# Optimization experiments

Measured on AMD Instinct MI355X. Metric: run time of the kernel, lower is better.

The kernel has to match this reference:

```python
import jax, jax.numpy as jnp
import numpy as np

N = 100000
E = 1600000
F_IN = 32   # node_features
F_H = 32    # filters
F_OUT = 4


def setup_inputs() -> dict:
    key = jax.random.key(0)
    ks = jax.random.split(key, 24)
    inp = {
        'x': jax.random.normal(ks[0], (N, F_IN), dtype=jnp.float32),
        'edge_index': jax.random.randint(ks[1], (2, E), 0, N, dtype=jnp.int64),
        'edge_weight': jax.random.uniform(ks[2], (E,), dtype=jnp.float32),
        'H': jax.random.normal(ks[3], (N, F_H), dtype=jnp.float32),
    }
    # ChebConv params: W[k] for k in {0,1} (K=2), bias per conv.
    def cheb_params(kw, kb, fin):
        s = 1.0 / np.sqrt(fin)
        W = jax.random.uniform(kw, (2, fin, F_H), jnp.float32, -s, s)
        b = jax.random.uniform(kb, (F_H,), jnp.float32, -s, s)
        return W, b
    names = ['xz', 'hz', 'xr', 'hr', 'xh', 'hh']
    fins = [F_IN, F_H, F_IN, F_H, F_IN, F_H]
    for i, (nm, fin) in enumerate(zip(names, fins)):
        W, b = cheb_params(ks[4 + 2 * i], ks[5 + 2 * i], fin)
        inp['W' + nm] = W
        inp['b' + nm] = b
    s = 1.0 / np.sqrt(F_H)
    inp['lin_w'] = jax.random.uniform(ks[20], (F_H, F_OUT), jnp.float32, -s, s)
    inp['lin_b'] = jax.random.uniform(ks[21], (F_OUT,), jnp.float32, -s, s)
    return inp


def _cheb(x, src, dst, nw, W, b):
    # ChebConv, K=2, sym norm, lambda_max=2 => L_hat = -D^{-1/2} A D^{-1/2}
    # (diagonal of scaled Laplacian cancels exactly: 1 - 1 = 0).
    tx1 = -jax.ops.segment_sum(nw[:, None] * x[src], dst, num_segments=N)
    return x @ W[0] + tx1 @ W[1] + b


def reference(x, edge_index, edge_weight, H,
              Wxz, bxz, Whz, bhz, Wxr, bxr, Whr, bhr, Wxh, bxh, Whh, bhh,
              lin_w, lin_b):
    src, dst = edge_index[0], edge_index[1]
    # remove_self_loops equivalent: zero out self-loop weights
    w = jnp.where(src == dst, 0.0, edge_weight)
    deg = jax.ops.segment_sum(w, src, num_segments=N)
    dinv = jnp.where(deg > 0, jax.lax.rsqrt(jnp.maximum(deg, 1e-30)), 0.0)
    nw = dinv[src] * w * dinv[dst]  # per-edge sym-normalized weight

    Z = jax.nn.sigmoid(_cheb(x, src, dst, nw, Wxz, bxz) +
                       _cheb(H, src, dst, nw, Whz, bhz))
    R = jax.nn.sigmoid(_cheb(x, src, dst, nw, Wxr, bxr) +
                       _cheb(H, src, dst, nw, Whr, bhr))
    H_tilde = jnp.tanh(_cheb(x, src, dst, nw, Wxh, bxh) +
                       _cheb(H * R, src, dst, nw, Whh, bhh))
    h = Z * H + (1.0 - Z) * H_tilde
    out = jax.nn.relu(h) @ lin_w + lin_b
    return (out, h)
```

## Files before the change

kernel.cpp:

```cpp
#include <hip/hip_runtime.h>
#include <hip/hip_bf16.h>
#include <hip/hip_fp16.h>

typedef __hip_bfloat16 bf16;
typedef __attribute__((ext_vector_type(8))) short bf16x8;
typedef __attribute__((ext_vector_type(4))) float f32x4;

#define NN   100000
#define EE   1600000
#define FH   32
#define FOUT 4
#define NBD  782
#define NBS  196
#define CAPB 2432
#define CAPS 8960
#define CAP  64
#define BINBLK 256
#define BINTHR 1024
#define EPB  6250
#define MFMA16(a, b, c) __builtin_amdgcn_mfma_f32_16x16x32_bf16(a, b, c, 0, 0, 0)

__device__ __forceinline__ float b2f(bf16 v) { return __bfloat162float(v); }

__device__ __forceinline__ float ldf(const void* p, int i, int f32) {
    return f32 ? ((const float*)p)[i] : b2f(((const bf16*)p)[i]);
}
__device__ __forceinline__ int ldi(const void* p, int i, int i64f) {
    return i64f ? (int)(((const long long*)p)[i]) : ((const int*)p)[i];
}
__device__ __forceinline__ void stf(void* p, int i, int f32, float v) {
    if (f32) ((float*)p)[i] = v;
    else     ((bf16*)p)[i] = __float2bfloat16(v);
}
__device__ __forceinline__ float h2f(unsigned short u) {
    return __half2float(__ushort_as_half(u));
}
__device__ __forceinline__ unsigned short f2h16(float v) {
    return __half_as_ushort(__float2half(v));
}
__device__ __forceinline__ short f2bf(float v) {
    unsigned u = __float_as_uint(v);
    return (short)((u + 0x7FFFu + ((u >> 16) & 1u)) >> 16);
}
__device__ __forceinline__ unsigned q8(float v) {
    int q = (int)rintf(v * 16.f) + 128;
    q = q < 0 ? 0 : (q > 255 ? 255 : q);
    return (unsigned)q;
}
__device__ __forceinline__ float ub(unsigned w, int k) {
    return (float)((w >> (k * 8)) & 0xFFu);
}
__device__ __forceinline__ float4 bfly_g(float4 v) {
    v.x += __shfl_xor(v.x, 8);  v.y += __shfl_xor(v.y, 8);
    v.z += __shfl_xor(v.z, 8);  v.w += __shfl_xor(v.w, 8);
    v.x += __shfl_xor(v.x, 16); v.y += __shfl_xor(v.y, 16);
    v.z += __shfl_xor(v.z, 16); v.w += __shfl_xor(v.w, 16);
    return v;
}
__device__ __forceinline__ bf16x8 bfragT(const short* __restrict__ wt, int idx) {
    return *(const bf16x8*)(wt + idx);
}

__global__ __launch_bounds__(256) void k_detect(const void* __restrict__ x,
                                                const void* __restrict__ ei,
                                                int* __restrict__ flg,
                                                int* __restrict__ binCur,
                                                int* __restrict__ binCurS) {
    __shared__ int s_f32[256], s_oddnz[256];
    int t = threadIdx.x;
    for (int i = t; i < NBD; i += 256) binCur[i] = i * CAPB;
    for (int i = t; i < NBS; i += 256) binCurS[i] = i * CAPS;
    float v = b2f(((const bf16*)x)[t]);
    s_f32[t] = (!isfinite(v)) || (fabsf(v) > 100.f);
    int w32 = ((const int*)ei)[t];
    s_oddnz[t] = ((t & 1) && (w32 != 0)) ? 1 : 0;
    __syncthreads();
    if (t == 0) {
        int f32 = 0, oddnz = 0;
        for (int i = 0; i < 256; i++) { f32 |= s_f32[i]; oddnz |= s_oddnz[i]; }
        flg[0] = f32;
        flg[1] = oddnz ? 0 : 1;
    }
}

__global__ __launch_bounds__(256) void k_prepw(
    const void* __restrict__ W0, const void* __restrict__ W1,
    const void* __restrict__ W2, const void* __restrict__ W3,
    const void* __restrict__ W4, const void* __restrict__ W5,
    const int* __restrict__ flg, short* __restrict__ wt) {
    int i = blockIdx.x * 256 + threadIdx.x;
    if (i >= 6 * 2048) return;
    int mat = i >> 11;
    int r = i & 2047;
    int cheb = r >> 10, k = (r >> 5) & 31, n = r & 31;
    const void* W = (mat == 0) ? W0 : (mat == 1) ? W1 : (mat == 2) ? W2
                  : (mat == 3) ? W3 : (mat == 4) ? W4 : W5;
    wt[(((mat << 1) + cheb) << 10) + n * 32 + k] = f2bf(ldf(W, r, flg[0]));
}

__global__ __launch_bounds__(256) void k_pack(const void* __restrict__ x,
                                              const void* __restrict__ H,
                                              const int* __restrict__ flg,
                                              unsigned* __restrict__ xh,
                                              unsigned short* __restrict__ xh8) {
    int i = blockIdx.x * 256 + threadIdx.x;
    if (i >= NN * FH) return;
    int f32 = flg[0];
    float xv = ldf(x, i, f32);
    float hv = ldf(H, i, f32);
    xh[i] = ((unsigned)f2h16(hv) << 16) | f2h16(xv);
    xh8[i] = (unsigned short)((q8(hv) << 8) | q8(xv));
}

__global__ __launch_bounds__(BINTHR) void k_bin(const void* __restrict__ ei,
                                                const void* __restrict__ ew,
                                                const int* __restrict__ flg,
                                                int* __restrict__ binCur,
                                                int* __restrict__ binCurS,
                                                int2* __restrict__ dstRec,
                                                int* __restrict__ srcRec) {
    __shared__ int hD[NBD], bD[NBD], lofD[NBD];
    __shared__ int hS[NBS], bS[NBS], lofS[NBS];
    __shared__ int sc[BINTHR];
    __shared__ int2 stD[EPB];
    __shared__ int  stS[EPB];
    int t = threadIdx.x;
    for (int i = t; i < NBD; i += BINTHR) hD[i] = 0;
    for (int i = t; i < NBS; i += BINTHR) hS[i] = 0;
    __syncthreads();
    int e0 = blockIdx.x * EPB;
    int e1 = e0 + EPB; if (e1 > EE) e1 = EE;
    int f32 = flg[0], i64 = flg[1];
    for (int e = e0 + t; e < e1; e += BINTHR) {
        int s = ldi(ei, e, i64);
        int d = ldi(ei, EE + e, i64);
        atomicAdd(&hD[d >> 7], 1);
        atomicAdd(&hS[s >> 9], 1);
    }
    __syncthreads();
    for (int i = t; i < NBD; i += BINTHR)
        bD[i] = (hD[i] > 0) ? atomicAdd(&binCur[i], hD[i]) : 0;
    for (int i = t; i < NBS; i += BINTHR)
        bS[i] = (hS[i] > 0) ? atomicAdd(&binCurS[i], hS[i]) : 0;
    int vD = (t < NBD) ? hD[t] : 0;
    sc[t] = vD;
    __syncthreads();
    for (int ofs = 1; ofs < BINTHR; ofs <<= 1) {
        int u = (t >= ofs) ? sc[t - ofs] : 0;
        __syncthreads();
        sc[t] += u;
        __syncthreads();
    }
    if (t < NBD) { lofD[t] = sc[t] - vD; hD[t] = 0; }
    __syncthreads();
    int vS = (t < NBS) ? hS[t] : 0;
    sc[t] = vS;
    __syncthreads();
    for (int ofs = 1; ofs < BINTHR; ofs <<= 1) {
        int u = (t >= ofs) ? sc[t - ofs] : 0;
        __syncthreads();
        sc[t] += u;
        __syncthreads();
    }
    if (t < NBS) { lofS[t] = sc[t] - vS; hS[t] = 0; }
    __syncthreads();
    for (int e = e0 + t; e < e1; e += BINTHR) {
        int s = ldi(ei, e, i64);
        int d = ldi(ei, EE + e, i64);
        float w = (s == d) ? 0.f : ldf(ew, e, f32);
        int wh = (int)(f2h16(w) & 0x7FFFu);
        int bd = d >> 7, bs = s >> 9;
        int rd = atomicAdd(&hD[bd], 1);
        int rs = atomicAdd(&hS[bs], 1);
        stD[lofD[bd] + rd] = make_int2((int)(((unsigned)s << 15) | wh),
                                       (bd << 8) | (d & 127));
        stS[lofS[bs] + rs] = (int)(((unsigned)bs << 24) |
                                   ((unsigned)(s & 511) << 15) | (unsigned)wh);
    }
    __syncthreads();
    int tot = e1 - e0;
    for (int i = t; i < tot; i += BINTHR) {
        int2 r = stD[i];
        int bin = ((unsigned)r.y) >> 8;
        int g = bD[bin] + (i - lofD[bin]);
        if (g < (bin + 1) * CAPB) dstRec[g] = make_int2(r.x, r.y & 127);
        int u = stS[i];
        int sbin = ((unsigned)u) >> 24;
        int gs = bS[sbin] + (i - lofS[sbin]);
        if (gs < (sbin + 1) * CAPS) srcRec[gs] = u & 0xFFFFFF;
    }
}

__global__ __launch_bounds__(256) void k_fillb(const int* __restrict__ binCur,
                                               const int2* __restrict__ dstRec,
                                               int* __restrict__ cursor,
                                               int* __restrict__ ell) {
    __shared__ int lCur[128];
    __shared__ int lEll[128 * CAP];
    int b = blockIdx.x, t = threadIdx.x;
    if (t < 128) lCur[t] = 0;
    __syncthreads();
    int cnt = binCur[b] - b * CAPB;
    if (cnt > CAPB) cnt = CAPB;
    for (int i = t; i < cnt; i += 256) {
        int2 r = dstRec[b * CAPB + i];
        int slot = atomicAdd(&lCur[r.y], 1);
        if (slot < CAP) lEll[r.y * CAP + slot] = r.x;
    }
    __syncthreads();
    int nodeBase = b * 128;
    for (int i = t; i < 128 * CAP; i += 256) {
        int node = nodeBase + (i >> 6);
        if (node < NN && (i & 63) < lCur[i >> 6])
            ell[(size_t)node * CAP + (i & (CAP - 1))] = lEll[i];
    }
    if (t < 128 && nodeBase + t < NN) {
        int c = lCur[t]; if (c > CAP) c = CAP;
        cursor[nodeBase + t] = c;
    }
}

__global__ __launch_bounds__(256) void k_degb(const int* __restrict__ binCurS,
                                              const int* __restrict__ srcRec,
                                              float* __restrict__ dinv) {
    __shared__ float lDeg[512];
    int b = blockIdx.x, t = threadIdx.x;
    lDeg[t] = 0.f; lDeg[t + 256] = 0.f;
    __syncthreads();
    int cnt = binCurS[b] - b * CAPS;
    if (cnt > CAPS) cnt = CAPS;
    for (int i = t; i < cnt; i += 256) {
        int r = srcRec[b * CAPS + i];
        atomicAdd(&lDeg[(r >> 15) & 511], h2f((unsigned short)(r & 0x7FFF)));
    }
    __syncthreads();
    #pragma unroll
    for (int k = 0; k < 2; k++) {
        int li = t + k * 256;
        int node = b * 512 + li;
        if (node < NN) {
            float dv = lDeg[li];
            dinv[node] = (dv > 0.f) ? rsqrtf(dv) : 0.f;
        }
    }
}

__global__ __launch_bounds__(256) void k_gather1(const int* __restrict__ cursor,
                                                 const int* __restrict__ ell,
                                                 const float* __restrict__ dinv,
                                                 const unsigned short* __restrict__ xh8,
                                                 unsigned* __restrict__ axah) {
    int t = threadIdx.x;
    int node = blockIdx.x * 8 + (t >> 5);
    if (node >= NN) return;
    int f = t & 31;
    int g = f >> 3, c = f & 7;
    int cnt = cursor[node];
    size_t base = (size_t)node * CAP;
    float4 ax = {0.f, 0.f, 0.f, 0.f}, ah = {0.f, 0.f, 0.f, 0.f};
    float cs = 0.f;
    for (int j = 0; j < cnt; j += 16) {
        int wrd[4]; float cf[4]; uint2 pv[4];
        #pragma unroll
        for (int u = 0; u < 4; u++) {
            int jj = j + u * 4 + g;
            wrd[u] = (jj < cnt) ? ell[base + jj] : 0;
        }
        #pragma unroll
        for (int u = 0; u < 4; u++) {
            int s = ((unsigned)wrd[u]) >> 15;
            cf[u] = dinv[s] * h2f((unsigned short)(wrd[u] & 0x7FFF));
            pv[u] = ((const uint2*)xh8)[s * 8 + c];
        }
        #pragma unroll
        for (int u = 0; u < 4; u++) {
            cs += cf[u];
            ax.x += cf[u] * ub(pv[u].x, 0);
            ah.x += cf[u] * ub(pv[u].x, 1);
            ax.y += cf[u] * ub(pv[u].x, 2);
            ah.y += cf[u] * ub(pv[u].x, 3);
            ax.z += cf[u] * ub(pv[u].y, 0);
            ah.z += cf[u] * ub(pv[u].y, 1);
            ax.w += cf[u] * ub(pv[u].y, 2);
            ah.w += cf[u] * ub(pv[u].y, 3);
        }
    }
    ax = bfly_g(ax); ah = bfly_g(ah);
    cs += __shfl_xor(cs, 8);
    cs += __shfl_xor(cs, 16);
    if (g == 0) {
        float dd = -dinv[node];
        float bias = 8.f * cs;
        uint4 o;
        o.x = ((unsigned)f2h16(dd * (ah.x * 0.0625f - bias)) << 16)
            | f2h16(dd * (ax.x * 0.0625f - bias));
        o.y = ((unsigned)f2h16(dd * (ah.y * 0.0625f - bias)) << 16)
            | f2h16(dd * (ax.y * 0.0625f - bias));
        o.z = ((unsigned)f2h16(dd * (ah.z * 0.0625f - bias)) << 16)
            | f2h16(dd * (ax.z * 0.0625f - bias));
        o.w = ((unsigned)f2h16(dd * (ah.w * 0.0625f - bias)) << 16)
            | f2h16(dd * (ax.w * 0.0625f - bias));
        ((uint4*)(axah + (size_t)node * FH))[c] = o;
    }
}

__global__ __launch_bounds__(256) void k_zr_mfma(
    const unsigned* __restrict__ xh, const unsigned* __restrict__ axah,
    const int* __restrict__ flg, const short* __restrict__ wt,
    const void* __restrict__ bxz, const void* __restrict__ bhz,
    const void* __restrict__ bxr, const void* __restrict__ bhr,
    float* __restrict__ Z, unsigned short* __restrict__ hr16) {
    int t = threadIdx.x;
    int lane = t & 63, wv = t >> 6;
    int f32 = flg[0];
    int c = lane & 15, quad = lane >> 4, kb = quad * 8;
    int nodeBase = blockIdx.x * 64 + wv * 16;
    int nm = nodeBase + c; if (nm >= NN) nm = NN - 1;

    bf16x8 fx, fHH, fAX, fAH;
    {
        const uint4* p = (const uint4*)(xh + (size_t)nm * FH + kb);
        uint4 a = p[0], b = p[1];
        unsigned wd[8] = {a.x, a.y, a.z, a.w, b.x, b.y, b.z, b.w};
        #pragma unroll
        for (int j = 0; j < 8; j++) {
            fx[j]  = f2bf(h2f((unsigned short)(wd[j] & 0xFFFF)));
            fHH[j] = f2bf(h2f((unsigned short)(wd[j] >> 16)));
        }
    }
    {
        const uint4* p = (const uint4*)(axah + (size_t)nm * FH + kb);
        uint4 a = p[0], b = p[1];
        unsigned wd[8] = {a.x, a.y, a.z, a.w, b.x, b.y, b.z, b.w};
        #pragma unroll
        for (int j = 0; j < 8; j++) {
            fAX[j] = f2bf(h2f((unsigned short)(wd[j] & 0xFFFF)));
            fAH[j] = f2bf(h2f((unsigned short)(wd[j] >> 16)));
        }
    }

    float bz0 = ldf(bxz, c, f32) + ldf(bhz, c, f32);
    float bz1 = ldf(bxz, c + 16, f32) + ldf(bhz, c + 16, f32);
    float br0 = ldf(bxr, c, f32) + ldf(bhr, c, f32);
    float br1 = ldf(bxr, c + 16, f32) + ldf(bhr, c + 16, f32);
    f32x4 az0 = {bz0, bz0, bz0, bz0}, az1 = {bz1, bz1, bz1, bz1};
    f32x4 ar0 = {br0, br0, br0, br0}, ar1 = {br1, br1, br1, br1};

    int i0 = c * 32 + kb;
    int i1 = (c + 16) * 32 + kb;
    az0 = MFMA16(fx,  bfragT(wt, 0 * 1024 + i0), az0);
    az0 = MFMA16(fAX, bfragT(wt, 1 * 1024 + i0), az0);
    az0 = MFMA16(fHH, bfragT(wt, 2 * 1024 + i0), az0);
    az0 = MFMA16(fAH, bfragT(wt, 3 * 1024 + i0), az0);
    az1 = MFMA16(fx,  bfragT(wt, 0 * 1024 + i1), az1);
    az1 = MFMA16(fAX, bfragT(wt, 1 * 1024 + i1), az1);
    az1 = MFMA16(fHH, bfragT(wt, 2 * 1024 + i1), az1);
    az1 = MFMA16(fAH, bfragT(wt, 3 * 1024 + i1), az1);
    ar0 = MFMA16(fx,  bfragT(wt, 4 * 1024 + i0), ar0);
    ar0 = MFMA16(fAX, bfragT(wt, 5 * 1024 + i0), ar0);
    ar0 = MFMA16(fHH, bfragT(wt, 6 * 1024 + i0), ar0);
    ar0 = MFMA16(fAH, bfragT(wt, 7 * 1024 + i0), ar0);
    ar1 = MFMA16(fx,  bfragT(wt, 4 * 1024 + i1), ar1);
    ar1 = MFMA16(fAX, bfragT(wt, 5 * 1024 + i1), ar1);
    ar1 = MFMA16(fHH, bfragT(wt, 6 * 1024 + i1), ar1);
    ar1 = MFMA16(fAH, bfragT(wt, 7 * 1024 + i1), ar1);

    #pragma unroll
    for (int tl = 0; tl < 2; tl++) {
        f32x4 az = tl ? az1 : az0, ar = tl ? ar1 : ar0;
        int f = c + 16 * tl;
        #pragma unroll
        for (int r = 0; r < 4; r++) {
            int node = nodeBase + quad * 4 + r;
            if (node < NN) {
                float zv = 1.f / (1.f + expf(-az[r]));
                float rv = 1.f / (1.f + expf(-ar[r]));
                float Hv = h2f((unsigned short)(xh[(size_t)node * FH + f] >> 16));
                Z[(size_t)node * FH + f] = zv;
                hr16[(size_t)node * FH + f] = f2h16(Hv * rv);
            }
        }
    }
}

__global__ __launch_bounds__(256) void k_gather2(const int* __restrict__ cursor,
                                                 const int* __restrict__ ell,
                                                 const float* __restrict__ dinv,
                                                 const unsigned short* __restrict__ hr16,
                                                 unsigned short* __restrict__ ahr16) {
    int t = threadIdx.x;
    int node = blockIdx.x * 8 + (t >> 5);
    if (node >= NN) return;
    int f = t & 31;
    int g = f >> 3, c = f & 7;
    int cnt = cursor[node];
    size_t base = (size_t)node * CAP;
    float4 acc = {0.f, 0.f, 0.f, 0.f};
    for (int j = 0; j < cnt; j += 8) {
        int jj0 = j + g, jj1 = j + 4 + g;
        int wrd0 = (jj0 < cnt) ? ell[base + jj0] : 0;
        int wrd1 = (jj1 < cnt) ? ell[base + jj1] : 0;
        int s0 = ((unsigned)wrd0) >> 15;
        int s1 = ((unsigned)wrd1) >> 15;
        float c0 = dinv[s0] * h2f((unsigned short)(wrd0 & 0x7FFF));
        float c1 = dinv[s1] * h2f((unsigned short)(wrd1 & 0x7FFF));
        ushort4 h0 = ((const ushort4*)hr16)[s0 * 8 + c];
        ushort4 h1 = ((const ushort4*)hr16)[s1 * 8 + c];
        acc.x += c0 * h2f(h0.x) + c1 * h2f(h1.x);
        acc.y += c0 * h2f(h0.y) + c1 * h2f(h1.y);
        acc.z += c0 * h2f(h0.z) + c1 * h2f(h1.z);
        acc.w += c0 * h2f(h0.w) + c1 * h2f(h1.w);
    }
    acc = bfly_g(acc);
    if (g == 0) {
        float dd = -dinv[node];
        ushort4 o = {f2h16(dd * acc.x), f2h16(dd * acc.y),
                     f2h16(dd * acc.z), f2h16(dd * acc.w)};
        ((ushort4*)(ahr16 + (size_t)node * FH))[c] = o;
    }
}

__global__ __launch_bounds__(256) void k_final_mfma(
    const unsigned* __restrict__ xh, const unsigned* __restrict__ axah,
    const int* __restrict__ flg, const short* __restrict__ wt,
    const float* __restrict__ Z, const unsigned short* __restrict__ hr16,
    const unsigned short* __restrict__ ahr16,
    const void* __restrict__ bxh, const void* __restrict__ bhh,
    const void* __restrict__ lin_w, const void* __restrict__ lin_b,
    void* __restrict__ out) {
    __shared__ float srh[64][FH];
    __shared__ float slw[FH * FOUT];
    __shared__ float slb[FOUT];

    int t = threadIdx.x;
    int lane = t & 63, wv = t >> 6;
    int f32 = flg[0];
    int c = lane & 15, quad = lane >> 4, kb = quad * 8;
    int nodeBase = blockIdx.x * 64 + wv * 16;
    int nm = nodeBase + c; if (nm >= NN) nm = NN - 1;

    if (t < FH * FOUT) slw[t] = ldf(lin_w, t, f32);
    if (t < FOUT) slb[t] = ldf(lin_b, t, f32);

    bf16x8 fx, fAX, fHR, fAHR;
    {
        const uint4* p = (const uint4*)(xh + (size_t)nm * FH + kb);
        uint4 a = p[0], b = p[1];
        unsigned wd[8] = {a.x, a.y, a.z, a.w, b.x, b.y, b.z, b.w};
        #pragma unroll
        for (int j = 0; j < 8; j++)
            fx[j] = f2bf(h2f((unsigned short)(wd[j] & 0xFFFF)));
    }
    {
        const uint4* p = (const uint4*)(axah + (size_t)nm * FH + kb);
        uint4 a = p[0], b = p[1];
        unsigned wd[8] = {a.x, a.y, a.z, a.w, b.x, b.y, b.z, b.w};
        #pragma unroll
        for (int j = 0; j < 8; j++)
            fAX[j] = f2bf(h2f((unsigned short)(wd[j] & 0xFFFF)));
    }
    {
        const uint4* p = (const uint4*)(hr16 + (size_t)nm * FH + kb);
        uint4 a = p[0];
        unsigned wd[4] = {a.x, a.y, a.z, a.w};
        #pragma unroll
        for (int j = 0; j < 8; j++)
            fHR[j] = f2bf(h2f((unsigned short)((wd[j >> 1] >> ((j & 1) * 16)) & 0xFFFF)));
    }
    {
        const uint4* p = (const uint4*)(ahr16 + (size_t)nm * FH + kb);
        uint4 a = p[0];
        unsigned wd[4] = {a.x, a.y, a.z, a.w};
        #pragma unroll
        for (int j = 0; j < 8; j++)
            fAHR[j] = f2bf(h2f((unsigned short)((wd[j >> 1] >> ((j & 1) * 16)) & 0xFFFF)));
    }

    float bh0 = ldf(bxh, c, f32) + ldf(bhh, c, f32);
    float bh1 = ldf(bxh, c + 16, f32) + ldf(bhh, c + 16, f32);
    f32x4 a0 = {bh0, bh0, bh0, bh0}, a1 = {bh1, bh1, bh1, bh1};

    int i0 = c * 32 + kb;
    int i1 = (c + 16) * 32 + kb;
    a0 = MFMA16(fx,   bfragT(wt,  8 * 1024 + i0), a0);
    a0 = MFMA16(fAX,  bfragT(wt,  9 * 1024 + i0), a0);
    a0 = MFMA16(fHR,  bfragT(wt, 10 * 1024 + i0), a0);
    a0 = MFMA16(fAHR, bfragT(wt, 11 * 1024 + i0), a0);
    a1 = MFMA16(fx,   bfragT(wt,  8 * 1024 + i1), a1);
    a1 = MFMA16(fAX,  bfragT(wt,  9 * 1024 + i1), a1);
    a1 = MFMA16(fHR,  bfragT(wt, 10 * 1024 + i1), a1);
    a1 = MFMA16(fAHR, bfragT(wt, 11 * 1024 + i1), a1);

    #pragma unroll
    for (int tl = 0; tl < 2; tl++) {
        f32x4 a = tl ? a1 : a0;
        int f = c + 16 * tl;
        #pragma unroll
        for (int r = 0; r < 4; r++) {
            int node = nodeBase + quad * 4 + r;
            if (node < NN) {
                float ht = tanhf(a[r]);
                float zv = Z[(size_t)node * FH + f];
                float Hv = h2f((unsigned short)(xh[(size_t)node * FH + f] >> 16));
                float hval = zv * Hv + (1.f - zv) * ht;
                stf(out, NN * FOUT + node * FH + f, f32, hval);
                srh[wv * 16 + quad * 4 + r][f] = hval > 0.f ? hval : 0.f;
            }
        }
    }
    __syncthreads();

    int nl = t >> 2, fo = t & 3;
    int node2 = blockIdx.x * 64 + nl;
    if (node2 < NN) {
        float acc = slb[fo];
        #pragma unroll
        for (int k = 0; k < FH; k++) acc += srh[nl][k] * slw[k * FOUT + fo];
        stf(out, node2 * FOUT + fo, f32, acc);
    }
}

extern "C" void kernel_launch(void* const* d_in, const int* in_sizes, int n_in,
                              void* d_out, int out_size, void* d_ws, size_t ws_size,
                              hipStream_t stream) {
    const void* x   = d_in[0];
    const void* ei  = d_in[1];
    const void* ew  = d_in[2];
    const void* H   = d_in[3];
    const void* Wxz = d_in[4];
    const void* bxz = d_in[5];
    const void* Whz = d_in[6];
    const void* bhz = d_in[7];
    const void* Wxr = d_in[8];
    const void* bxr = d_in[9];
    const void* Whr = d_in[10];
    const void* bhr = d_in[11];
    const void* Wxh = d_in[12];
    const void* bxh = d_in[13];
    const void* Whh = d_in[14];
    const void* bhh = d_in[15];
    const void* lnw = d_in[16];
    const void* lnb = d_in[17];

    char* base = (char*)d_ws;
    int*            flg     = (int*)base;            base += 64;
    int*            binCur  = (int*)base;            base += (NBD * 4 + 63) & ~63;
    int*            binCurS = (int*)base;            base += (NBS * 4 + 63) & ~63;
    float*          dinv    = (float*)base;          base += (size_t)NN * 4;
    int*            cursor  = (int*)base;            base += (size_t)NN * 4;
    short*          wt      = (short*)base;          base += (12288 * 2 + 63) & ~63;
    unsigned*       xh      = (unsigned*)base;       base += (size_t)NN * FH * 4;
    unsigned short* xh8     = (unsigned short*)base; base += (size_t)NN * FH * 2;
    char*           aliasRg = base;
    unsigned*       axah    = (unsigned*)base;       base += (size_t)NN * FH * 4;
    float*          Z       = (float*)base;          base += (size_t)NN * FH * 4;
    unsigned short* hr16    = (unsigned short*)base; base += (size_t)NN * FH * 2;
    unsigned short* ahr16   = (unsigned short*)base; base += (size_t)NN * FH * 2;
    int*            ell     = (int*)base;
    int2*           dstRec  = (int2*)aliasRg;
    int*            srcRec  = (int*)(aliasRg + (size_t)NBD * CAPB * 8);

    const int pb   = (NN * FH + 255) / 256;
    const int n8b  = (NN + 7) / 8;
    const int n64b = (NN + 63) / 64;

    k_detect<<<1, 256, 0, stream>>>(x, ei, flg, binCur, binCurS);
    k_prepw<<<48, 256, 0, stream>>>(Wxz, Whz, Wxr, Whr, Wxh, Whh, flg, wt);
    k_pack<<<pb, 256, 0, stream>>>(x, H, flg, xh, xh8);
    k_bin<<<BINBLK, BINTHR, 0, stream>>>(ei, ew, flg, binCur, binCurS,
                                         dstRec, srcRec);
    k_fillb<<<NBD, 256, 0, stream>>>(binCur, dstRec, cursor, ell);
    k_degb<<<NBS, 256, 0, stream>>>(binCurS, srcRec, dinv);
    k_gather1<<<n8b, 256, 0, stream>>>(cursor, ell, dinv, xh8, axah);
    k_zr_mfma<<<n64b, 256, 0, stream>>>(xh, axah, flg, wt,
                                        bxz, bhz, bxr, bhr, Z, hr16);
    k_gather2<<<n8b, 256, 0, stream>>>(cursor, ell, dinv, hr16, ahr16);
    k_final_mfma<<<n64b, 256, 0, stream>>>(xh, axah, flg, wt, Z, hr16, ahr16,
                                           bxh, bhh, lnw, lnb, d_out);
}
```

Measured before the change: 272.5 us.

## Fuse ELL build, first gather and Z/R MFMA; fuse second gather with final MFMA

Merges detect, weight prep and packing into a single prep kernel. The ELL bucket fill, the first neighbour aggregation and the Z/R MFMA stage now run in one kernel that keeps adjacency and aggregates in shared memory. The second gather is fused into the final MFMA kernel. Z is stored as fp16 instead of fp32, and the bin scan uses wave shuffles instead of a barrier-heavy LDS scan. This cuts launches and global round-trips of intermediates, but the fused gather kernel uses more shared memory (lower occupancy), and the aliased workspace region is split into separate buffers.

Measured after the change: 292.7 us. 1.07x slower.

```diff
diff --git a/kernel.cpp b/kernel.cpp
--- a/kernel.cpp
+++ b/kernel.cpp
@@ -61,55 +61,49 @@
     return *(const bf16x8*)(wt + idx);
 }
 
-__global__ __launch_bounds__(256) void k_detect(const void* __restrict__ x,
-                                                const void* __restrict__ ei,
-                                                int* __restrict__ flg,
-                                                int* __restrict__ binCur,
-                                                int* __restrict__ binCurS) {
-    __shared__ int s_f32[256], s_oddnz[256];
-    int t = threadIdx.x;
-    for (int i = t; i < NBD; i += 256) binCur[i] = i * CAPB;
-    for (int i = t; i < NBS; i += 256) binCurS[i] = i * CAPS;
-    float v = b2f(((const bf16*)x)[t]);
-    s_f32[t] = (!isfinite(v)) || (fabsf(v) > 100.f);
-    int w32 = ((const int*)ei)[t];
-    s_oddnz[t] = ((t & 1) && (w32 != 0)) ? 1 : 0;
-    __syncthreads();
-    if (t == 0) {
-        int f32 = 0, oddnz = 0;
-        for (int i = 0; i < 256; i++) { f32 |= s_f32[i]; oddnz |= s_oddnz[i]; }
-        flg[0] = f32;
-        flg[1] = oddnz ? 0 : 1;
-    }
-}
-
-__global__ __launch_bounds__(256) void k_prepw(
+__global__ __launch_bounds__(256) void k_prep(
+    const void* __restrict__ x, const void* __restrict__ H,
+    const void* __restrict__ ei,
     const void* __restrict__ W0, const void* __restrict__ W1,
     const void* __restrict__ W2, const void* __restrict__ W3,
     const void* __restrict__ W4, const void* __restrict__ W5,
-    const int* __restrict__ flg, short* __restrict__ wt) {
-    int i = blockIdx.x * 256 + threadIdx.x;
-    if (i >= 6 * 2048) return;
-    int mat = i >> 11;
-    int r = i & 2047;
-    int cheb = r >> 10, k = (r >> 5) & 31, n = r & 31;
-    const void* W = (mat == 0) ? W0 : (mat == 1) ? W1 : (mat == 2) ? W2
-                  : (mat == 3) ? W3 : (mat == 4) ? W4 : W5;
-    wt[(((mat << 1) + cheb) << 10) + n * 32 + k] = f2bf(ldf(W, r, flg[0]));
-}
-
-__global__ __launch_bounds__(256) void k_pack(const void* __restrict__ x,
-                                              const void* __restrict__ H,
-                                              const int* __restrict__ flg,
-                                              unsigned* __restrict__ xh,
-                                              unsigned short* __restrict__ xh8) {
-    int i = blockIdx.x * 256 + threadIdx.x;
-    if (i >= NN * FH) return;
-    int f32 = flg[0];
-    float xv = ldf(x, i, f32);
-    float hv = ldf(H, i, f32);
-    xh[i] = ((unsigned)f2h16(hv) << 16) | f2h16(xv);
-    xh8[i] = (unsigned short)((q8(hv) << 8) | q8(xv));
+    int* __restrict__ flg, int* __restrict__ binCur, int* __restrict__ binCurS,
+    short* __restrict__ wt, unsigned* __restrict__ xh,
+    unsigned short* __restrict__ xh8) {
+    __shared__ int s_fl[2];
+    int t = threadIdx.x, b = blockIdx.x;
+    if (t == 0) { s_fl[0] = 0; s_fl[1] = 0; }
+    __syncthreads();
+    {
+        float v = b2f(((const bf16*)x)[t]);
+        if ((!isfinite(v)) || (fabsf(v) > 100.f)) atomicOr(&s_fl[0], 1);
+        int w32 = ((const int*)ei)[t];
+        if ((t & 1) && (w32 != 0)) atomicOr(&s_fl[1], 1);
+    }
+    __syncthreads();
+    int f32 = s_fl[0];
+    int i64 = s_fl[1] ? 0 : 1;
+    if (b == 0 && t == 0) { flg[0] = f32; flg[1] = i64; }
+    if (b < 48) {
+        int i = b * 256 + t;
+        int mat = i >> 11;
+        int r = i & 2047;
+        int cheb = r >> 10, k = (r >> 5) & 31, n = r & 31;
+        const void* W = (mat == 0) ? W0 : (mat == 1) ? W1 : (mat == 2) ? W2
+                      : (mat == 3) ? W3 : (mat == 4) ? W4 : W5;
+        wt[(((mat << 1) + cheb) << 10) + n * 32 + k] = f2bf(ldf(W, r, f32));
+    } else if (b == 48) {
+        for (int i = t; i < NBD; i += 256) binCur[i] = i * CAPB;
+    } else if (b == 49) {
+        for (int i = t; i < NBS; i += 256) binCurS[i] = i * CAPS;
+    }
+    int i = b * 256 + t;
+    if (i < NN * FH) {
+        float xv = ldf(x, i, f32);
+        float hv = ldf(H, i, f32);
+        xh[i] = ((unsigned)f2h16(hv) << 16) | f2h16(xv);
+        xh8[i] = (unsigned short)((q8(hv) << 8) | q8(xv));
+    }
 }
 
 __global__ __launch_bounds__(BINTHR) void k_bin(const void* __restrict__ ei,
@@ -121,10 +115,11 @@
                                                 int* __restrict__ srcRec) {
     __shared__ int hD[NBD], bD[NBD], lofD[NBD];
     __shared__ int hS[NBS], bS[NBS], lofS[NBS];
-    __shared__ int sc[BINTHR];
+    __shared__ int sWave[16];
     __shared__ int2 stD[EPB];
     __shared__ int  stS[EPB];
     int t = threadIdx.x;
+    int lane = t & 63, wv = t >> 6;
     for (int i = t; i < NBD; i += BINTHR) hD[i] = 0;
     for (int i = t; i < NBS; i += BINTHR) hS[i] = 0;
     __syncthreads();
@@ -143,26 +138,54 @@
     for (int i = t; i < NBS; i += BINTHR)
         bS[i] = (hS[i] > 0) ? atomicAdd(&binCurS[i], hS[i]) : 0;
     int vD = (t < NBD) ? hD[t] : 0;
-    sc[t] = vD;
-    __syncthreads();
-    for (int ofs = 1; ofs < BINTHR; ofs <<= 1) {
-        int u = (t >= ofs) ? sc[t - ofs] : 0;
-        __syncthreads();
-        sc[t] += u;
-        __syncthreads();
-    }
-    if (t < NBD) { lofD[t] = sc[t] - vD; hD[t] = 0; }
+    int p = vD;
+    #pragma unroll
+    for (int ofs = 1; ofs < 64; ofs <<= 1) {
+        int u = __shfl_up(p, ofs);
+        if (lane >= ofs) p += u;
+    }
+    if (lane == 63) sWave[wv] = p;
+    __syncthreads();
+    if (t < 16) {
+        int q = sWave[t];
+        #pragma unroll
+        for (int ofs = 1; ofs < 16; ofs <<= 1) {
+            int u = __shfl_up(q, ofs);
+            if (t >= ofs) q += u;
+        }
+        sWave[t] = q;
+    }
+    __syncthreads();
+    if (t < NBD) {
+        int incl = p + (wv ? sWave[wv - 1] : 0);
+        lofD[t] = incl - vD;
+        hD[t] = 0;
+    }
     __syncthreads();
     int vS = (t < NBS) ? hS[t] : 0;
-    sc[t] = vS;
-    __syncthreads();
-    for (int ofs = 1; ofs < BINTHR; ofs <<= 1) {
-        int u = (t >= ofs) ? sc[t - ofs] : 0;
-        __syncthreads();
-        sc[t] += u;
-        __syncthreads();
-    }
-    if (t < NBS) { lofS[t] = sc[t] - vS; hS[t] = 0; }
+    p = vS;
+    #pragma unroll
+    for (int ofs = 1; ofs < 64; ofs <<= 1) {
+        int u = __shfl_up(p, ofs);
+        if (lane >= ofs) p += u;
+    }
+    if (lane == 63) sWave[wv] = p;
+    __syncthreads();
+    if (t < 16) {
+        int q = sWave[t];
+        #pragma unroll
+        for (int ofs = 1; ofs < 16; ofs <<= 1) {
+            int u = __shfl_up(q, ofs);
+            if (t >= ofs) q += u;
+        }
+        sWave[t] = q;
+    }
+    __syncthreads();
+    if (t < NBS) {
+        int incl = p + (wv ? sWave[wv - 1] : 0);
+        lofS[t] = incl - vS;
+        hS[t] = 0;
+    }
     __syncthreads();
     for (int e = e0 + t; e < e1; e += BINTHR) {
         int s = ldi(ei, e, i64);
@@ -191,35 +214,6 @@
     }
 }
 
-__global__ __launch_bounds__(256) void k_fillb(const int* __restrict__ binCur,
-                                               const int2* __restrict__ dstRec,
-                                               int* __restrict__ cursor,
-                                               int* __restrict__ ell) {
-    __shared__ int lCur[128];
-    __shared__ int lEll[128 * CAP];
-    int b = blockIdx.x, t = threadIdx.x;
-    if (t < 128) lCur[t] = 0;
-    __syncthreads();
-    int cnt = binCur[b] - b * CAPB;
-    if (cnt > CAPB) cnt = CAPB;
-    for (int i = t; i < cnt; i += 256) {
-        int2 r = dstRec[b * CAPB + i];
-        int slot = atomicAdd(&lCur[r.y], 1);
-        if (slot < CAP) lEll[r.y * CAP + slot] = r.x;
-    }
-    __syncthreads();
-    int nodeBase = b * 128;
-    for (int i = t; i < 128 * CAP; i += 256) {
-        int node = nodeBase + (i >> 6);
-        if (node < NN && (i & 63) < lCur[i >> 6])
-            ell[(size_t)node * CAP + (i & (CAP - 1))] = lEll[i];
-    }
-    if (t < 128 && nodeBase + t < NN) {
-        int c = lCur[t]; if (c > CAP) c = CAP;
-        cursor[nodeBase + t] = c;
-    }
-}
-
 __global__ __launch_bounds__(256) void k_degb(const int* __restrict__ binCurS,
                                               const int* __restrict__ srcRec,
                                               float* __restrict__ dinv) {
@@ -245,243 +239,269 @@
     }
 }
 
-__global__ __launch_bounds__(256) void k_gather1(const int* __restrict__ cursor,
-                                                 const int* __restrict__ ell,
-                                                 const float* __restrict__ dinv,
-                                                 const unsigned short* __restrict__ xh8,
-                                                 unsigned* __restrict__ axah) {
-    int t = threadIdx.x;
-    int node = blockIdx.x * 8 + (t >> 5);
-    if (node >= NN) return;
-    int f = t & 31;
-    int g = f >> 3, c = f & 7;
-    int cnt = cursor[node];
-    size_t base = (size_t)node * CAP;
-    float4 ax = {0.f, 0.f, 0.f, 0.f}, ah = {0.f, 0.f, 0.f, 0.f};
-    float cs = 0.f;
-    for (int j = 0; j < cnt; j += 16) {
-        int wrd[4]; float cf[4]; uint2 pv[4];
-        #pragma unroll
-        for (int u = 0; u < 4; u++) {
-            int jj = j + u * 4 + g;
-            wrd[u] = (jj < cnt) ? ell[base + jj] : 0;
-        }
-        #pragma unroll
-        for (int u = 0; u < 4; u++) {
-            int s = ((unsigned)wrd[u]) >> 15;
-            cf[u] = dinv[s] * h2f((unsigned short)(wrd[u] & 0x7FFF));
-            pv[u] = ((const uint2*)xh8)[s * 8 + c];
-        }
-        #pragma unroll
-        for (int u = 0; u < 4; u++) {
-            cs += cf[u];
-            ax.x += cf[u] * ub(pv[u].x, 0);
-            ah.x += cf[u] * ub(pv[u].x, 1);
-            ax.y += cf[u] * ub(pv[u].x, 2);
-            ah.y += cf[u] * ub(pv[u].x, 3);
-            ax.z += cf[u] * ub(pv[u].y, 0);
-            ah.z += cf[u] * ub(pv[u].y, 1);
-            ax.w += cf[u] * ub(pv[u].y, 2);
-            ah.w += cf[u] * ub(pv[u].y, 3);
-        }
-    }
-    ax = bfly_g(ax); ah = bfly_g(ah);
-    cs += __shfl_xor(cs, 8);
-    cs += __shfl_xor(cs, 16);
-    if (g == 0) {
-        float dd = -dinv[node];
-        float bias = 8.f * cs;
-        uint4 o;
-        o.x = ((unsigned)f2h16(dd * (ah.x * 0.0625f - bias)) << 16)
-            | f2h16(dd * (ax.x * 0.0625f - bias));
-        o.y = ((unsigned)f2h16(dd * (ah.y * 0.0625f - bias)) << 16)
-            | f2h16(dd * (ax.y * 0.0625f - bias));
-        o.z = ((unsigned)f2h16(dd * (ah.z * 0.0625f - bias)) << 16)
-            | f2h16(dd * (ax.z * 0.0625f - bias));
-        o.w = ((unsigned)f2h16(dd * (ah.w * 0.0625f - bias)) << 16)
-            | f2h16(dd * (ax.w * 0.0625f - bias));
-        ((uint4*)(axah + (size_t)node * FH))[c] = o;
-    }
-}
-
-__global__ __launch_bounds__(256) void k_zr_mfma(
+__global__ __launch_bounds__(256) void k_fgz(
+    const int* __restrict__ binCur, const int2* __restrict__ dstRec,
+    const float* __restrict__ dinv, const unsigned short* __restrict__ xh8,
+    const unsigned* __restrict__ xh, const int* __restrict__ flg,
+    const short* __restrict__ wt,
+    const void* __restrict__ bxz, const void* __restrict__ bhz,
+    const void* __restrict__ bxr, const void* __restrict__ bhr,
+    int* __restrict__ cursor, int* __restrict__ ell,
+    unsigned* __restrict__ axah, unsigned short* __restrict__ zf16,
+    unsigned short* __restrict__ hr16) {
+    __shared__ int lCur[128];
+    __shared__ int lEll[128 * CAP];
+    __shared__ unsigned sAX[128][33];
+    int b = blockIdx.x, t = threadIdx.x;
+    if (t < 128) lCur[t] = 0;
+    __syncthreads();
+    int cnt = binCur[b] - b * CAPB;
+    if (cnt > CAPB) cnt = CAPB;
+    for (int i = t; i < cnt; i += 256) {
+        int2 r = dstRec[b * CAPB + i];
+        int slot = atomicAdd(&lCur[r.y], 1);
+        if (slot < CAP) lEll[r.y * CAP + slot] = r.x;
+    }
+    __syncthreads();
+    int nodeBase = b * 128;
+    for (int i = t; i < 128 * CAP; i += 256) {
+        int node = nodeBase + (i >> 6);
+        if (node < NN && (i & 63) < lCur[i >> 6])
+            ell[(size_t)node * CAP + (i & 63)] = lEll[i];
+    }
+    if (t < 128 && nodeBase + t < NN) {
+        int c2 = lCur[t]; if (c2 > CAP) c2 = CAP;
+        cursor[nodeBase + t] = c2;
+    }
+    int gg = t >> 5, f = t & 31, g = f >> 3, c = f & 7;
+    for (int pass = 0; pass < 16; pass++) {
+        int ln = pass * 8 + gg;
+        int node = nodeBase + ln;
+        if (node >= NN) continue;
+        int cnt2 = lCur[ln]; if (cnt2 > CAP) cnt2 = CAP;
+        int base = ln * CAP;
+        float4 ax = {0.f, 0.f, 0.f, 0.f}, ah = {0.f, 0.f, 0.f, 0.f};
+        float cs = 0.f;
+        for (int j = 0; j < cnt2; j += 16) {
+            int wrd[4]; float cf[4]; uint2 pv[4];
+            #pragma unroll
+            for (int u = 0; u < 4; u++) {
+                int jj = j + u * 4 + g;
+                wrd[u] = (jj < cnt2) ? lEll[base + jj] : 0;
+            }
+            #pragma unroll
+            for (int u = 0; u < 4; u++) {
+                int s = ((unsigned)wrd[u]) >> 15;
+                cf[u] = dinv[s] * h2f((unsigned short)(wrd[u] & 0x7FFF));
+                pv[u] = ((const uint2*)xh8)[s * 8 + c];
+            }
+            #pragma unroll
+            for (int u = 0; u < 4; u++) {
+                cs += cf[u];
+                ax.x += cf[u] * ub(pv[u].x, 0);
+                ah.x += cf[u] * ub(pv[u].x, 1);
+                ax.y += cf[u] * ub(pv[u].x, 2);
+                ah.y += cf[u] * ub(pv[u].x, 3);
+                ax.z += cf[u] * ub(pv[u].y, 0);
+                ah.z += cf[u] * ub(pv[u].y, 1);
+                ax.w += cf[u] * ub(pv[u].y, 2);
+                ah.w += cf[u] * ub(pv[u].y, 3);
+            }
+        }
+        ax = bfly_g(ax); ah = bfly_g(ah);
+        cs += __shfl_xor(cs, 8);
+        cs += __shfl_xor(cs, 16);
+        if (g == 0) {
+            float dd = -dinv[node];
+            float bias = 8.f * cs;
+            uint4 o;
+            o.x = ((unsigned)f2h16(dd * (ah.x * 0.0625f - bias)) << 16)
+                | f2h16(dd * (ax.x * 0.0625f - bias));
+            o.y = ((unsigned)f2h16(dd * (ah.y * 0.0625f - bias)) << 16)
+                | f2h16(dd * (ax.y * 0.0625f - bias));
+            o.z = ((unsigned)f2h16(dd * (ah.z * 0.0625f - bias)) << 16)
+                | f2h16(dd * (ax.z * 0.0625f - bias));
+            o.w = ((unsigned)f2h16(dd * (ah.w * 0.0625f - bias)) << 16)
+                | f2h16(dd * (ax.w * 0.0625f - bias));
+            sAX[ln][4 * c + 0] = o.x;
+            sAX[ln][4 * c + 1] = o.y;
+            sAX[ln][4 * c + 2] = o.z;
+            sAX[ln][4 * c + 3] = o.w;
+            ((uint4*)(axah + (size_t)node * FH))[c] = o;
+        }
+    }
+    __syncthreads();
+    int lane = t & 63, wv = t >> 6;
+    int fl32 = flg[0];
+    int cc = lane & 15, quad = lane >> 4, kb = quad * 8;
+    float bz0 = ldf(bxz, cc, fl32) + ldf(bhz, cc, fl32);
+    float bz1 = ldf(bxz, cc + 16, fl32) + ldf(bhz, cc + 16, fl32);
+    float br0 = ldf(bxr, cc, fl32) + ldf(bhr, cc, fl32);
+    float br1 = ldf(bxr, cc + 16, fl32) + ldf(bhr, cc + 16, fl32);
+    for (int half = 0; half < 2; half++) {
+        int nb2 = nodeBase + half * 64 + wv * 16;
+        int nm = nb2 + cc; if (nm >= NN) nm = NN - 1;
+        int lm = nm - nodeBase;
+        bf16x8 fx, fHH, fAX, fAH;
+        {
+            const uint4* p = (const uint4*)(xh + (size_t)nm * FH + kb);
+            uint4 aa = p[0], bb = p[1];
+            unsigned wd[8] = {aa.x, aa.y, aa.z, aa.w, bb.x, bb.y, bb.z, bb.w};
+            #pragma unroll
+            for (int j = 0; j < 8; j++) {
+                fx[j]  = f2bf(h2f((unsigned short)(wd[j] & 0xFFFF)));
+                fHH[j] = f2bf(h2f((unsigned short)(wd[j] >> 16)));
+            }
+        }
+        {
+            unsigned wd[8];
+            #pragma unroll
+            for (int j = 0; j < 8; j++) wd[j] = sAX[lm][kb + j];
+            #pragma unroll
+            for (int j = 0; j < 8; j++) {
+                fAX[j] = f2bf(h2f((unsigned short)(wd[j] & 0xFFFF)));
+                fAH[j] = f2bf(h2f((unsigned short)(wd[j] >> 16)));
+            }
+        }
+        f32x4 az0 = {bz0, bz0, bz0, bz0}, az1 = {bz1, bz1, bz1, bz1};
+        f32x4 ar0 = {br0, br0, br0, br0}, ar1 = {br1, br1, br1, br1};
+        int i0 = cc * 32 + kb;
+        int i1 = (cc + 16) * 32 + kb;
+        az0 = MFMA16(fx,  bfragT(wt, 0 * 1024 + i0), az0);
+        az0 = MFMA16(fAX, bfragT(wt, 1 * 1024 + i0), az0);
+        az0 = MFMA16(fHH, bfragT(wt, 2 * 1024 + i0), az0);
+        az0 = MFMA16(fAH, bfragT(wt, 3 * 1024 + i0), az0);
+        az1 = MFMA16(fx,  bfragT(wt, 0 * 1024 + i1), az1);
+        az1 = MFMA16(fAX, bfragT(wt, 1 * 1024 + i1), az1);
+        az1 = MFMA16(fHH, bfragT(wt, 2 * 1024 + i1), az1);
+        az1 = MFMA16(fAH, bfragT(wt, 3 * 1024 + i1), az1);
+        ar0 = MFMA16(fx,  bfragT(wt, 4 * 1024 + i0), ar0);
+        ar0 = MFMA16(fAX, bfragT(wt, 5 * 1024 + i0), ar0);
+        ar0 = MFMA16(fHH, bfragT(wt, 6 * 1024 + i0), ar0);
+        ar0 = MFMA16(fAH, bfragT(wt, 7 * 1024 + i0), ar0);
+        ar1 = MFMA16(fx,  bfragT(wt, 4 * 1024 + i1), ar1);
+        ar1 = MFMA16(fAX, bfragT(wt, 5 * 1024 + i1), ar1);
+        ar1 = MFMA16(fHH, bfragT(wt, 6 * 1024 + i1), ar1);
+        ar1 = MFMA16(fAH, bfragT(wt, 7 * 1024 + i1), ar1);
+        #pragma unroll
+        for (int tl = 0; tl < 2; tl++) {
+            f32x4 az = tl ? az1 : az0, ar = tl ? ar1 : ar0;
+            int ff = cc + 16 * tl;
+            #pragma unroll
+            for (int r = 0; r < 4; r++) {
+                int node = nb2 + quad * 4 + r;
+                if (node < NN) {
+                    float zv = 1.f / (1.f + expf(-az[r]));
+                    float rv = 1.f / (1.f + expf(-ar[r]));
+                    float Hv = h2f((unsigned short)(xh[(size_t)node * FH + ff] >> 16));
+                    zf16[(size_t)node * FH + ff] = f2h16(zv);
+                    hr16[(size_t)node * FH + ff] = f2h16(Hv * rv);
+                }
+            }
+        }
+    }
+}
+
+__global__ __launch_bounds__(256) void k_fgf(
+    const int* __restrict__ cursor, const int* __restrict__ ell,
+    const float* __restrict__ dinv, const unsigned short* __restrict__ hr16,
     const unsigned* __restrict__ xh, const unsigned* __restrict__ axah,
     const int* __restrict__ flg, const short* __restrict__ wt,
-    const void* __restrict__ bxz, const void* __restrict__ bhz,
-    const void* __restrict__ bxr, const void* __restrict__ bhr,
-    float* __restrict__ Z, unsigned short* __restrict__ hr16) {
-    int t = threadIdx.x;
-    int lane = t & 63, wv = t >> 6;
-    int f32 = flg[0];
-    int c = lane & 15, quad = lane >> 4, kb = quad * 8;
-    int nodeBase = blockIdx.x * 64 + wv * 16;
-    int nm = nodeBase + c; if (nm >= NN) nm = NN - 1;
-
-    bf16x8 fx, fHH, fAX, fAH;
-    {
-        const uint4* p = (const uint4*)(xh + (size_t)nm * FH + kb);
-        uint4 a = p[0], b = p[1];
-        unsigned wd[8] = {a.x, a.y, a.z, a.w, b.x, b.y, b.z, b.w};
-        #pragma unroll
-        for (int j = 0; j < 8; j++) {
-            fx[j]  = f2bf(h2f((unsigned short)(wd[j] & 0xFFFF)));
-            fHH[j] = f2bf(h2f((unsigned short)(wd[j] >> 16)));
-        }
-    }
-    {
-        const uint4* p = (const uint4*)(axah + (size_t)nm * FH + kb);
-        uint4 a = p[0], b = p[1];
-        unsigned wd[8] = {a.x, a.y, a.z, a.w, b.x, b.y, b.z, b.w};
-        #pragma unroll
-        for (int j = 0; j < 8; j++) {
-            fAX[j] = f2bf(h2f((unsigned short)(wd[j] & 0xFFFF)));
-            fAH[j] = f2bf(h2f((unsigned short)(wd[j] >> 16)));
-        }
-    }
-
-    float bz0 = ldf(bxz, c, f32) + ldf(bhz, c, f32);
-    float bz1 = ldf(bxz, c + 16, f32) + ldf(bhz, c + 16, f32);
-    float br0 = ldf(bxr, c, f32) + ldf(bhr, c, f32);
-    float br1 = ldf(bxr, c + 16, f32) + ldf(bhr, c + 16, f32);
-    f32x4 az0 = {bz0, bz0, bz0, bz0}, az1 = {bz1, bz1, bz1, bz1};
-    f32x4 ar0 = {br0, br0, br0, br0}, ar1 = {br1, br1, br1, br1};
-
-    int i0 = c * 32 + kb;
-    int i1 = (c + 16) * 32 + kb;
-    az0 = MFMA16(fx,  bfragT(wt, 0 * 1024 + i0), az0);
-    az0 = MFMA16(fAX, bfragT(wt, 1 * 1024 + i0), az0);
-    az0 = MFMA16(fHH, bfragT(wt, 2 * 1024 + i0), az0);
-    az0 = MFMA16(fAH, bfragT(wt, 3 * 1024 + i0), az0);
-    az1 = MFMA16(fx,  bfragT(wt, 0 * 1024 + i1), az1);
-    az1 = MFMA16(fAX, bfragT(wt, 1 * 1024 + i1), az1);
-    az1 = MFMA16(fHH, bfragT(wt, 2 * 1024 + i1), az1);
-    az1 = MFMA16(fAH, bfragT(wt, 3 * 1024 + i1), az1);
-    ar0 = MFMA16(fx,  bfragT(wt, 4 * 1024 + i0), ar0);
-    ar0 = MFMA16(fAX, bfragT(wt, 5 * 1024 + i0), ar0);
-    ar0 = MFMA16(fHH, bfragT(wt, 6 * 1024 + i0), ar0);
-    ar0 = MFMA16(fAH, bfragT(wt, 7 * 1024 + i0), ar0);
-    ar1 = MFMA16(fx,  bfragT(wt, 4 * 1024 + i1), ar1);
-    ar1 = MFMA16(fAX, bfragT(wt, 5 * 1024 + i1), ar1);
-    ar1 = MFMA16(fHH, bfragT(wt, 6 * 1024 + i1), ar1);
-    ar1 = MFMA16(fAH, bfragT(wt, 7 * 1024 + i1), ar1);
-
-    #pragma unroll
-    for (int tl = 0; tl < 2; tl++) {
-        f32x4 az = tl ? az1 : az0, ar = tl ? ar1 : ar0;
-        int f = c + 16 * tl;
-        #pragma unroll
-        for (int r = 0; r < 4; r++) {
-            int node = nodeBase + quad * 4 + r;
-            if (node < NN) {
-                float zv = 1.f / (1.f + expf(-az[r]));
-                float rv = 1.f / (1.f + expf(-ar[r]));
-                float Hv = h2f((unsigned short)(xh[(size_t)node * FH + f] >> 16));
-                Z[(size_t)node * FH + f] = zv;
-                hr16[(size_t)node * FH + f] = f2h16(Hv * rv);
-            }
-        }
-    }
-}
-
-__global__ __launch_bounds__(256) void k_gather2(const int* __restrict__ cursor,
-                                                 const int* __restrict__ ell,
-                                                 const float* __restrict__ dinv,
-                                                 const unsigned short* __restrict__ hr16,
-                                                 unsigned short* __restrict__ ahr16) {
-    int t = threadIdx.x;
-    int node = blockIdx.x * 8 + (t >> 5);
-    if (node >= NN) return;
-    int f = t & 31;
-    int g = f >> 3, c = f & 7;
-    int cnt = cursor[node];
-    size_t base = (size_t)node * CAP;
-    float4 acc = {0.f, 0.f, 0.f, 0.f};
-    for (int j = 0; j < cnt; j += 8) {
-        int jj0 = j + g, jj1 = j + 4 + g;
-        int wrd0 = (jj0 < cnt) ? ell[base + jj0] : 0;
-        int wrd1 = (jj1 < cnt) ? ell[base + jj1] : 0;
-        int s0 = ((unsigned)wrd0) >> 15;
-        int s1 = ((unsigned)wrd1) >> 15;
-        float c0 = dinv[s0] * h2f((unsigned short)(wrd0 & 0x7FFF));
-        float c1 = dinv[s1] * h2f((unsigned short)(wrd1 & 0x7FFF));
-        ushort4 h0 = ((const ushort4*)hr16)[s0 * 8 + c];
-        ushort4 h1 = ((const ushort4*)hr16)[s1 * 8 + c];
-        acc.x += c0 * h2f(h0.x) + c1 * h2f(h1.x);
-        acc.y += c0 * h2f(h0.y) + c1 * h2f(h1.y);
-        acc.z += c0 * h2f(h0.z) + c1 * h2f(h1.z);
-        acc.w += c0 * h2f(h0.w) + c1 * h2f(h1.w);
-    }
-    acc = bfly_g(acc);
-    if (g == 0) {
-        float dd = -dinv[node];
-        ushort4 o = {f2h16(dd * acc.x), f2h16(dd * acc.y),
-                     f2h16(dd * acc.z), f2h16(dd * acc.w)};
-        ((ushort4*)(ahr16 + (size_t)node * FH))[c] = o;
-    }
-}
-
-__global__ __launch_bounds__(256) void k_final_mfma(
-    const unsigned* __restrict__ xh, const unsigned* __restrict__ axah,
-    const int* __restrict__ flg, const short* __restrict__ wt,
-    const float* __restrict__ Z, const unsigned short* __restrict__ hr16,
-    const unsigned short* __restrict__ ahr16,
+    const unsigned short* __restrict__ zf16,
     const void* __restrict__ bxh, const void* __restrict__ bhh,
     const void* __restrict__ lin_w, const void* __restrict__ lin_b,
     void* __restrict__ out) {
+    __shared__ unsigned sAHR[64][17];
     __shared__ float srh[64][FH];
     __shared__ float slw[FH * FOUT];
     __shared__ float slb[FOUT];
-
-    int t = threadIdx.x;
-    int lane = t & 63, wv = t >> 6;
+    int b = blockIdx.x, t = threadIdx.x;
     int f32 = flg[0];
-    int c = lane & 15, quad = lane >> 4, kb = quad * 8;
-    int nodeBase = blockIdx.x * 64 + wv * 16;
-    int nm = nodeBase + c; if (nm >= NN) nm = NN - 1;
-
     if (t < FH * FOUT) slw[t] = ldf(lin_w, t, f32);
     if (t < FOUT) slb[t] = ldf(lin_b, t, f32);
-
+    int nodeBase = b * 64;
+    int gg = t >> 5, f = t & 31, g = f >> 3, c = f & 7;
+    for (int pass = 0; pass < 8; pass++) {
+        int ln = pass * 8 + gg;
+        int node = nodeBase + ln;
+        if (node >= NN) continue;
+        int cnt = cursor[node];
+        size_t base = (size_t)node * CAP;
+        float4 acc = {0.f, 0.f, 0.f, 0.f};
+        for (int j = 0; j < cnt; j += 16) {
+            int wrd[4]; float cf[4]; ushort4 hv[4];
+            #pragma unroll
+            for (int u = 0; u < 4; u++) {
+                int jj = j + u * 4 + g;
+                wrd[u] = (jj < cnt) ? ell[base + jj] : 0;
+            }
+            #pragma unroll
+            for (int u = 0; u < 4; u++) {
+                int s = ((unsigned)wrd[u]) >> 15;
+                cf[u] = dinv[s] * h2f((unsigned short)(wrd[u] & 0x7FFF));
+                hv[u] = ((const ushort4*)hr16)[s * 8 + c];
+            }
+            #pragma unroll
+            for (int u = 0; u < 4; u++) {
+                acc.x += cf[u] * h2f(hv[u].x);
+                acc.y += cf[u] * h2f(hv[u].y);
+                acc.z += cf[u] * h2f(hv[u].z);
+                acc.w += cf[u] * h2f(hv[u].w);
+            }
+        }
+        acc = bfly_g(acc);
+        if (g == 0) {
+            float dd = -dinv[node];
+            sAHR[ln][2 * c + 0] = ((unsigned)f2h16(dd * acc.y) << 16)
+                                | f2h16(dd * acc.x);
+            sAHR[ln][2 * c + 1] = ((unsigned)f2h16(dd * acc.w) << 16)
+                                | f2h16(dd * acc.z);
+        }
+    }
+    __syncthreads();
+    int lane = t & 63, wv = t >> 6;
+    int cc = lane & 15, quad = lane >> 4, kb = quad * 8;
+    int nb2 = nodeBase + wv * 16;
+    int nm = nb2 + cc; if (nm >= NN) nm = NN - 1;
+    int lm = nm - nodeBase;
     bf16x8 fx, fAX, fHR, fAHR;
     {
         const uint4* p = (const uint4*)(xh + (size_t)nm * FH + kb);
-        uint4 a = p[0], b = p[1];
-        unsigned wd[8] = {a.x, a.y, a.z, a.w, b.x, b.y, b.z, b.w};
+        uint4 aa = p[0], bb = p[1];
+        unsigned wd[8] = {aa.x, aa.y, aa.z, aa.w, bb.x, bb.y, bb.z, bb.w};
         #pragma unroll
         for (int j = 0; j < 8; j++)
             fx[j] = f2bf(h2f((unsigned short)(wd[j] & 0xFFFF)));
     }
     {
         const uint4* p = (const uint4*)(axah + (size_t)nm * FH + kb);
-        uint4 a = p[0], b = p[1];
-        unsigned wd[8] = {a.x, a.y, a.z, a.w, b.x, b.y, b.z, b.w};
+        uint4 aa = p[0], bb = p[1];
+        unsigned wd[8] = {aa.x, aa.y, aa.z, aa.w, bb.x, bb.y, bb.z, bb.w};
         #pragma unroll
         for (int j = 0; j < 8; j++)
             fAX[j] = f2bf(h2f((unsigned short)(wd[j] & 0xFFFF)));
     }
     {
         const uint4* p = (const uint4*)(hr16 + (size_t)nm * FH + kb);
-        uint4 a = p[0];
-        unsigned wd[4] = {a.x, a.y, a.z, a.w};
+        uint4 aa = p[0];
+        unsigned wd[4] = {aa.x, aa.y, aa.z, aa.w};
         #pragma unroll
         for (int j = 0; j < 8; j++)
             fHR[j] = f2bf(h2f((unsigned short)((wd[j >> 1] >> ((j & 1) * 16)) & 0xFFFF)));
     }
     {
-        const uint4* p = (const uint4*)(ahr16 + (size_t)nm * FH + kb);
-        uint4 a = p[0];
-        unsigned wd[4] = {a.x, a.y, a.z, a.w};
+        unsigned wd[4];
+        #pragma unroll
+        for (int m = 0; m < 4; m++) wd[m] = sAHR[lm][kb / 2 + m];
         #pragma unroll
         for (int j = 0; j < 8; j++)
             fAHR[j] = f2bf(h2f((unsigned short)((wd[j >> 1] >> ((j & 1) * 16)) & 0xFFFF)));
     }
-
-    float bh0 = ldf(bxh, c, f32) + ldf(bhh, c, f32);
-    float bh1 = ldf(bxh, c + 16, f32) + ldf(bhh, c + 16, f32);
+    float bh0 = ldf(bxh, cc, f32) + ldf(bhh, cc, f32);
+    float bh1 = ldf(bxh, cc + 16, f32) + ldf(bhh, cc + 16, f32);
     f32x4 a0 = {bh0, bh0, bh0, bh0}, a1 = {bh1, bh1, bh1, bh1};
-
-    int i0 = c * 32 + kb;
-    int i1 = (c + 16) * 32 + kb;
+    int i0 = cc * 32 + kb;
+    int i1 = (cc + 16) * 32 + kb;
     a0 = MFMA16(fx,   bfragT(wt,  8 * 1024 + i0), a0);
     a0 = MFMA16(fAX,  bfragT(wt,  9 * 1024 + i0), a0);
     a0 = MFMA16(fHR,  bfragT(wt, 10 * 1024 + i0), a0);
@@ -490,28 +510,26 @@
     a1 = MFMA16(fAX,  bfragT(wt,  9 * 1024 + i1), a1);
     a1 = MFMA16(fHR,  bfragT(wt, 10 * 1024 + i1), a1);
     a1 = MFMA16(fAHR, bfragT(wt, 11 * 1024 + i1), a1);
-
     #pragma unroll
     for (int tl = 0; tl < 2; tl++) {
         f32x4 a = tl ? a1 : a0;
-        int f = c + 16 * tl;
+        int ff = cc + 16 * tl;
         #pragma unroll
         for (int r = 0; r < 4; r++) {
-            int node = nodeBase + quad * 4 + r;
+            int node = nb2 + quad * 4 + r;
             if (node < NN) {
                 float ht = tanhf(a[r]);
-                float zv = Z[(size_t)node * FH + f];
-                float Hv = h2f((unsigned short)(xh[(size_t)node * FH + f] >> 16));
+                float zv = h2f(zf16[(size_t)node * FH + ff]);
+                float Hv = h2f((unsigned short)(xh[(size_t)node * FH + ff] >> 16));
                 float hval = zv * Hv + (1.f - zv) * ht;
-                stf(out, NN * FOUT + node * FH + f, f32, hval);
-                srh[wv * 16 + quad * 4 + r][f] = hval > 0.f ? hval : 0.f;
-            }
-        }
-    }
-    __syncthreads();
-
+                stf(out, NN * FOUT + node * FH + ff, f32, hval);
+                srh[node - nodeBase][ff] = hval > 0.f ? hval : 0.f;
+            }
+        }
+    }
+    __syncthreads();
     int nl = t >> 2, fo = t & 3;
-    int node2 = blockIdx.x * 64 + nl;
+    int node2 = nodeBase + nl;
     if (node2 < NN) {
         float acc = slb[fo];
         #pragma unroll
@@ -551,30 +569,24 @@
     short*          wt      = (short*)base;          base += (12288 * 2 + 63) & ~63;
     unsigned*       xh      = (unsigned*)base;       base += (size_t)NN * FH * 4;
     unsigned short* xh8     = (unsigned short*)base; base += (size_t)NN * FH * 2;
-    char*           aliasRg = base;
     unsigned*       axah    = (unsigned*)base;       base += (size_t)NN * FH * 4;
-    float*          Z       = (float*)base;          base += (size_t)NN * FH * 4;
+    unsigned short* zf16    = (unsigned short*)base; base += (size_t)NN * FH * 2;
     unsigned short* hr16    = (unsigned short*)base; base += (size_t)NN * FH * 2;
-    unsigned short* ahr16   = (unsigned short*)base; base += (size_t)NN * FH * 2;
-    int*            ell     = (int*)base;
-    int2*           dstRec  = (int2*)aliasRg;
-    int*            srcRec  = (int*)(aliasRg + (size_t)NBD * CAPB * 8);
+    int*            ell     = (int*)base;            base += (size_t)NN * CAP * 4;
+    int2*           dstRec  = (int2*)base;           base += (size_t)NBD * CAPB * 8;
+    int*            srcRec  = (int*)base;
 
     const int pb   = (NN * FH + 255) / 256;
-    const int n8b  = (NN + 7) / 8;
     const int n64b = (NN + 63) / 64;
 
-    k_detect<<<1, 256, 0, stream>>>(x, ei, flg, binCur, binCurS);
-    k_prepw<<<48, 256, 0, stream>>>(Wxz, Whz, Wxr, Whr, Wxh, Whh, flg, wt);
-    k_pack<<<pb, 256, 0, stream>>>(x, H, flg, xh, xh8);
+    k_prep<<<pb, 256, 0, stream>>>(x, H, ei, Wxz, Whz, Wxr, Whr, Wxh, Whh,
+                                   flg, binCur, binCurS, wt, xh, xh8);
     k_bin<<<BINBLK, BINTHR, 0, stream>>>(ei, ew, flg, binCur, binCurS,
                                          dstRec, srcRec);
-    k_fillb<<<NBD, 256, 0, stream>>>(binCur, dstRec, cursor, ell);
     k_degb<<<NBS, 256, 0, stream>>>(binCurS, srcRec, dinv);
-    k_gather1<<<n8b, 256, 0, stream>>>(cursor, ell, dinv, xh8, axah);
-    k_zr_mfma<<<n64b, 256, 0, stream>>>(xh, axah, flg, wt,
-                                        bxz, bhz, bxr, bhr, Z, hr16);
-    k_gather2<<<n8b, 256, 0, stream>>>(cursor, ell, dinv, hr16, ahr16);
-    k_final_mfma<<<n64b, 256, 0, stream>>>(xh, axah, flg, wt, Z, hr16, ahr16,
-                                           bxh, bhh, lnw, lnb, d_out);
-}
+    k_fgz<<<NBD, 256, 0, stream>>>(binCur, dstRec, dinv, xh8, xh, flg, wt,
+                                   bxz, bhz, bxr, bhr,
+                                   cursor, ell, axah, zf16, hr16);
+    k_fgf<<<n64b, 256, 0, stream>>>(cursor, ell, dinv, hr16, xh, axah, flg, wt,
+                                    zf16, bxh, bhh, lnw, lnb, d_out);
+}
```
